# Kernel optimization log

Measured on AMD Instinct MI355X. Metric: run time of the kernel, lower is better.

Reference implementation:

```python
import math
import jax, jax.numpy as jnp
import numpy as np

EMBED_DIM = 1024
NUM_HEADS = 16
HEAD_DIM = EMBED_DIM // NUM_HEADS
B, S = 4, 2048


def setup_inputs() -> dict:
    key = jax.random.key(0)
    ks = jax.random.split(key, 12)
    sc = 1.0 / math.sqrt(EMBED_DIM)
    inp = {
        "query": jax.random.normal(ks[0], (B, S, EMBED_DIM), jnp.float32),
        "key": jax.random.normal(ks[1], (B, S, EMBED_DIM), jnp.float32),
        "value": jax.random.normal(ks[2], (B, S, EMBED_DIM), jnp.float32),
        # causal mask: True = masked (upper triangle above diagonal)
        "attn_mask": jnp.triu(jnp.ones((S, S), jnp.bool_), k=1),
        "q_w": jax.random.normal(ks[3], (EMBED_DIM, EMBED_DIM), jnp.float32) * sc,
        "q_b": jax.random.normal(ks[4], (EMBED_DIM,), jnp.float32) * sc,
        "k_w": jax.random.normal(ks[5], (EMBED_DIM, EMBED_DIM), jnp.float32) * sc,
        "k_b": jax.random.normal(ks[6], (EMBED_DIM,), jnp.float32) * sc,
        "v_w": jax.random.normal(ks[7], (EMBED_DIM, EMBED_DIM), jnp.float32) * sc,
        "v_b": jax.random.normal(ks[8], (EMBED_DIM,), jnp.float32) * sc,
        "o_w": jax.random.normal(ks[9], (EMBED_DIM, EMBED_DIM), jnp.float32) * sc,
        "o_b": jax.random.normal(ks[10], (EMBED_DIM,), jnp.float32) * sc,
    }
    return inp


def _split_heads(x):
    # (B, S, E) -> (B, H, S, D)
    b, s, _ = x.shape
    return x.reshape(b, s, NUM_HEADS, HEAD_DIM).transpose(0, 2, 1, 3)


def reference(query, key, value, attn_mask, q_w, q_b, k_w, k_b, v_w, v_b, o_w, o_b):
    # torch Linear: y = x @ W.T + b
    q = _split_heads(query @ q_w.T + q_b)
    k = _split_heads(key @ k_w.T + k_b)
    v = _split_heads(value @ v_w.T + v_b)
    scale = math.sqrt(HEAD_DIM)
    scores = jnp.einsum("bhqd,bhkd->bhqk", q, k) / scale
    scores = jnp.where(attn_mask[None, None, :, :], -jnp.inf, scores)
    attn = jax.nn.softmax(scores, axis=-1)
    ctx = jnp.einsum("bhqk,bhkd->bhqd", attn, v)  # (B,H,S,D)
    ctx = ctx.transpose(0, 2, 1, 3).reshape(query.shape[0], query.shape[1], EMBED_DIM)
    return ctx @ o_w.T + o_b
```

## Files before the change

kernel.cpp:

```cpp
#include <hip/hip_runtime.h>
#include <stdint.h>

#define BB 4
#define SS 2048
#define EE 1024
#define HH 16
#define DD 64
#define MM (BB*SS)

typedef unsigned short u16;
typedef __attribute__((ext_vector_type(8))) short bf16x8;
typedef __attribute__((ext_vector_type(4))) float f32x4;

#define MFMA __builtin_amdgcn_mfma_f32_16x16x32_bf16

#if __has_builtin(__builtin_amdgcn_exp2f)
#define EXP2(x) __builtin_amdgcn_exp2f(x)
#else
#define EXP2(x) exp2f(x)
#endif

__device__ __forceinline__ u16 f2bf(float f) {
  union { float f; uint32_t u; } x; x.f = f;
  uint32_t r = (x.u + 0x7fffu + ((x.u >> 16) & 1u)) >> 16;
  return (u16)r;
}

__device__ __forceinline__ uint32_t cvtpk(float lo, float hi) {
  uint32_t r;
  asm volatile("v_cvt_pk_bf16_f32 %0, %1, %2" : "=v"(r) : "v"(lo), "v"(hi));
  return r;
}

__device__ __forceinline__ void gl_lds16(const void* g, void* l) {
  __builtin_amdgcn_global_load_lds(
      (const __attribute__((address_space(1))) uint32_t*)g,
      (__attribute__((address_space(3))) uint32_t*)l, 16, 0, 0);
}

__global__ __launch_bounds__(256) void cast_w(
    const float* __restrict__ s0, const float* __restrict__ s1,
    const float* __restrict__ s2, const float* __restrict__ s3,
    u16* __restrict__ d0, u16* __restrict__ d1,
    u16* __restrict__ d2, u16* __restrict__ d3) {
  int i = blockIdx.x * 256 + threadIdx.x;
  int sel = i >> 17, off = i & ((1 << 17) - 1);
  const float* s = sel == 0 ? s0 : sel == 1 ? s1 : sel == 2 ? s2 : s3;
  u16* d = sel == 0 ? d0 : sel == 1 ? d1 : sel == 2 ? d2 : d3;
  const float4* sp = (const float4*)s;
  float4 a = sp[off*2], b = sp[off*2+1];
  union { u16 h[8]; uint4 v; } o;
  o.h[0]=f2bf(a.x); o.h[1]=f2bf(a.y); o.h[2]=f2bf(a.z); o.h[3]=f2bf(a.w);
  o.h[4]=f2bf(b.x); o.h[5]=f2bf(b.y); o.h[6]=f2bf(b.z); o.h[7]=f2bf(b.w);
  *(uint4*)(d + (size_t)off*8) = o.v;
}

template<int A_FP32, int OUT_BF16>
__device__ __forceinline__ void gemm_body(
    const void* __restrict__ Ap, const u16* __restrict__ W,
    const float* __restrict__ bias, void* __restrict__ Cout,
    int Ndim, int Kdim, float scale, int m0, int n0,
    char* AsB, char* BsB) {
  const int tid = threadIdx.x;
  const int lane = tid & 63, w = tid >> 6;
  const int wr = w >> 1, wc = w & 1;
  const int l15 = lane & 15, l4 = lane >> 4;

  f32x4 acc[4][4] = {};

  const int br = tid >> 3, bsl = tid & 7;
  const int ar = tid >> 4, asl = tid & 15;

  auto stage = [&](int k0) {
    if (A_FP32) {
      const float* Af = (const float*)Ap;
      #pragma unroll
      for (int i = 0; i < 8; ++i) {
        int row = i*16 + ar;
        int ss = asl ^ (row & 7);
        gl_lds16(Af + (size_t)(m0 + row)*Kdim + k0 + ss*4, AsB + i*4096 + tid*16);
      }
    } else {
      const u16* Ah = (const u16*)Ap;
      #pragma unroll
      for (int i = 0; i < 4; ++i) {
        int row = i*32 + br;
        int ss = bsl ^ (row & 7);
        gl_lds16(Ah + (size_t)(m0 + row)*Kdim + k0 + ss*8, AsB + i*4096 + tid*16);
      }
    }
    #pragma unroll
    for (int i = 0; i < 4; ++i) {
      int row = i*32 + br;
      int ss = bsl ^ (row & 7);
      gl_lds16(W + (size_t)(n0 + row)*Kdim + k0 + ss*8, BsB + i*4096 + tid*16);
    }
  };

  for (int k0 = 0; k0 < Kdim; k0 += 64) {
    stage(k0);
    __syncthreads();

    bf16x8 af[2][4], bfr[2][4];
    #pragma unroll
    for (int m = 0; m < 4; ++m) {
      int r = wr*64 + m*16 + l15;
      if (A_FP32) {
        const char* rb = AsB + r*256;
        #pragma unroll
        for (int kk = 0; kk < 2; ++kk) {
          f32x4 fa = *(const f32x4*)(rb + (kk*8 + ((l4*2    ) ^ (r & 7)))*16);
          f32x4 fb = *(const f32x4*)(rb + (kk*8 + ((l4*2 + 1) ^ (r & 7)))*16);
          union { uint32_t u[4]; bf16x8 v; } cv;
          cv.u[0] = cvtpk(fa[0], fa[1]);
          cv.u[1] = cvtpk(fa[2], fa[3]);
          cv.u[2] = cvtpk(fb[0], fb[1]);
          cv.u[3] = cvtpk(fb[2], fb[3]);
          af[kk][m] = cv.v;
        }
      } else {
        const char* rb = AsB + r*128;
        #pragma unroll
        for (int kk = 0; kk < 2; ++kk)
          af[kk][m] = *(const bf16x8*)(rb + ((kk*4 + l4) ^ (r & 7))*16);
      }
    }
    #pragma unroll
    for (int n = 0; n < 4; ++n) {
      int rr = wc*64 + n*16 + l15;
      const char* rb = BsB + rr*128;
      #pragma unroll
      for (int kk = 0; kk < 2; ++kk)
        bfr[kk][n] = *(const bf16x8*)(rb + ((kk*4 + l4) ^ (rr & 7))*16);
    }
    #pragma unroll
    for (int kk = 0; kk < 2; ++kk)
      #pragma unroll
      for (int m = 0; m < 4; ++m)
        #pragma unroll
        for (int n = 0; n < 4; ++n)
          acc[m][n] = MFMA(af[kk][m], bfr[kk][n], acc[m][n], 0, 0, 0);
    __syncthreads();
  }

  const int ccol = wc*64 + l15;
  float bv[4];
  #pragma unroll
  for (int n = 0; n < 4; ++n) bv[n] = bias[n0 + ccol + n*16];
  #pragma unroll
  for (int m = 0; m < 4; ++m) {
    #pragma unroll
    for (int i = 0; i < 4; ++i) {
      size_t row = (size_t)(m0 + wr*64 + m*16 + l4*4 + i);
      #pragma unroll
      for (int n = 0; n < 4; ++n) {
        float v = (acc[m][n][i] + bv[n]) * scale;
        size_t idx = row * Ndim + (n0 + ccol + n*16);
        if (OUT_BF16) ((u16*)Cout)[idx] = f2bf(v);
        else          ((float*)Cout)[idx] = v;
      }
    }
  }
}

__global__ __launch_bounds__(256, 2) void gemm_qkv(
    const float* __restrict__ qx, const float* __restrict__ kx, const float* __restrict__ vx,
    const u16* __restrict__ wqm, const u16* __restrict__ wkm, const u16* __restrict__ wvm,
    const float* __restrict__ qbv, const float* __restrict__ kbv, const float* __restrict__ vbv,
    u16* __restrict__ qo, u16* __restrict__ ko, u16* __restrict__ vo) {
  __shared__ alignas(16) char AsB[32768];
  __shared__ alignas(16) char BsB[16384];
  const int flat = blockIdx.x + blockIdx.y * 8 + blockIdx.z * 512;
  const int j = flat & 7, s = flat >> 3;
  const int c = 6*j + (s >> 5), i = s & 31;
  const int nx = i & 7;
  const int my = ((c & 15) << 2) + (i >> 3);
  const int z = c >> 4;
  const float* A = z == 0 ? qx : z == 1 ? kx : vx;
  const u16* W = z == 0 ? wqm : z == 1 ? wkm : wvm;
  const float* bias = z == 0 ? qbv : z == 1 ? kbv : vbv;
  u16* C = z == 0 ? qo : z == 1 ? ko : vo;
  const float scale = z == 0 ? 0.125f : 1.0f;
  gemm_body<1,1>(A, W, bias, C, EE, EE, scale, my * 128, nx * 128, AsB, BsB);
}

__global__ __launch_bounds__(256, 4) void gemm_out(
    const u16* __restrict__ A, const u16* __restrict__ W,
    const float* __restrict__ bias, float* __restrict__ Cout) {
  __shared__ alignas(16) char AsB[16384];
  __shared__ alignas(16) char BsB[16384];
  const int flat = blockIdx.x + blockIdx.y * 8;
  const int j = flat & 7, s = flat >> 3;
  const int nx = s & 7, yy = (j << 3) + (s >> 3);
  gemm_body<0,0>(A, W, bias, Cout, EE, EE, 1.0f, yy * 128, nx * 128, AsB, BsB);
}

__global__ __launch_bounds__(256, 2) void attn10(
    const u16* __restrict__ Q, const u16* __restrict__ K,
    const u16* __restrict__ V, u16* __restrict__ ctx) {
  __shared__ alignas(16) u16 Ks[2][2][64*64];
  __shared__ alignas(16) u16 VTs[2][2][64*64];
  __shared__ alignas(16) u16 Ps[4][32*64];

  const int tid = threadIdx.x, lane = tid & 63, w = tid >> 6;
  const int l15 = lane & 15, l4 = lane >> 4;

  const int f = blockIdx.x;
  const int j = f & 7, s = f >> 3;
  const int qlo = s & 7;
  const int panel = j * 8 + (s >> 3);
  const int h = panel & 15, b = panel >> 4;
  const size_t base = ((size_t)b * SS) * EE + h * DD;

  const int kr  = tid >> 3;
  const int ksl = tid & 7;
  const int rv  = tid >> 2;
  const int vc  = tid & 3;

  u16* KsE  = (u16*)Ks;
  u16* VTsE = (u16*)VTs;
  u16* PsE  = (u16*)Ps + w * 2048;

  auto stageK = [&](int t, int pb, int sub) {
    #pragma unroll
    for (int i = 0; i < 2; ++i) {
      int row = i*32 + kr;
      gl_lds16(K + base + (size_t)(t*64 + row)*EE + (ksl ^ (row & 7))*8,
               KsE + pb*8192 + sub*4096 + i*2048 + tid*8);
    }
  };
  auto vtWrite = [&](int pb, int sub, bf16x8 v0, bf16x8 v1) {
    #pragma unroll
    for (int jj = 0; jj < 16; ++jj) {
      u16 val = jj < 8 ? (u16)v0[jj] : (u16)v1[jj - 8];
      int d = vc*16 + jj;
      int sl = (rv >> 3) ^ (jj & 7) ^ (vc << 1);
      VTsE[pb*8192 + sub*4096 + d*64 + sl*8 + (rv & 7)] = val;
    }
  };

  #pragma unroll 1
  for (int pass = 0; pass < 2; ++pass) {
    const int qblk = pass == 0 ? (15 - qlo) : qlo;
    const int q0 = qblk * 128, wq = q0 + w * 32;
    const int npairs = qblk + 1;

    bf16x8 qf[2][2];
    #pragma unroll
    for (int G = 0; G < 2; ++G)
      #pragma unroll
      for (int kc = 0; kc < 2; ++kc)
        qf[G][kc] = *(const bf16x8*)(Q + base + (size_t)(wq + G*16 + l15)*EE + kc*32 + l4*8);

    f32x4 o[2][4] = {};
    float lsum[2] = {0.f, 0.f};

    auto computeTile = [&](int t, int pb, int sub) {
      if (wq + 31 < t*64) return;
      const bool g0act = (wq + 15 >= t*64);
      const u16* tileK = KsE + pb*8192 + sub*4096;
      const u16* tileV = VTsE + pb*8192 + sub*4096;

      f32x4 sc[2][4] = {};
      __builtin_amdgcn_s_setprio(1);
      #pragma unroll
      for (int nt = 0; nt < 4; ++nt) {
        int row = nt*16 + l15;
        int sw = row & 7;
        const u16* kb = tileK + row*64;
        bf16x8 kf0 = *(const bf16x8*)(kb + ((l4    ) ^ sw)*8);
        bf16x8 kf1 = *(const bf16x8*)(kb + ((4 + l4) ^ sw)*8);
        sc[1][nt] = MFMA(kf0, qf[1][0], sc[1][nt], 0, 0, 0);
        sc[1][nt] = MFMA(kf1, qf[1][1], sc[1][nt], 0, 0, 0);
        if (g0act) {
          sc[0][nt] = MFMA(kf0, qf[0][0], sc[0][nt], 0, 0, 0);
          sc[0][nt] = MFMA(kf1, qf[0][1], sc[0][nt], 0, 0, 0);
        }
      }
      __builtin_amdgcn_s_setprio(0);

      #pragma unroll
      for (int G = 0; G < 2; ++G) {
        if (G == 0 && !g0act) continue;
        const bool nomask = (t*64 + 63 <= wq + G*16);
        const int qg = wq + G*16 + l15;
        #pragma unroll
        for (int nt = 0; nt < 4; ++nt) {
          float p0 = EXP2(__builtin_fmaf(sc[G][nt][0], 1.44269504f, -17.3123405f));
          float p1 = EXP2(__builtin_fmaf(sc[G][nt][1], 1.44269504f, -17.3123405f));
          float p2 = EXP2(__builtin_fmaf(sc[G][nt][2], 1.44269504f, -17.3123405f));
          float p3 = EXP2(__builtin_fmaf(sc[G][nt][3], 1.44269504f, -17.3123405f));
          if (!nomask) {
            int kvs = t*64 + nt*16 + l4*4;
            if (kvs + 0 > qg) p0 = 0.f;
            if (kvs + 1 > qg) p1 = 0.f;
            if (kvs + 2 > qg) p2 = 0.f;
            if (kvs + 3 > qg) p3 = 0.f;
          }
          lsum[G] += (p0 + p1) + (p2 + p3);
          uint2 pk;
          pk.x = cvtpk(p0, p1);
          pk.y = cvtpk(p2, p3);
          *(uint2*)((char*)PsE + (G*16 + l15)*128
                        + (((nt*2 + (l4 >> 1)) ^ (l15 & 7)) * 16)
                        + (l4 & 1) * 8) = pk;
        }
      }

      __builtin_amdgcn_s_setprio(1);
      #pragma unroll
      for (int cc = 0; cc < 2; ++cc) {
        bf16x8 pf1 = *(const bf16x8*)((char*)PsE + (16 + l15)*128
                                     + (((cc*4 + l4) ^ (l15 & 7)) * 16));
        bf16x8 pf0;
        if (g0act)
          pf0 = *(const bf16x8*)((char*)PsE + l15*128
                                     + (((cc*4 + l4) ^ (l15 & 7)) * 16));
        #pragma unroll
        for (int dm = 0; dm < 4; ++dm) {
          int sl = (cc*4 + l4) ^ (l15 & 7) ^ (dm << 1);
          bf16x8 vfv = *(const bf16x8*)(tileV + (dm*16 + l15)*64 + sl*8);
          o[1][dm] = MFMA(pf1, vfv, o[1][dm], 0, 0, 0);
          if (g0act) o[0][dm] = MFMA(pf0, vfv, o[0][dm], 0, 0, 0);
        }
      }
      __builtin_amdgcn_s_setprio(0);
    };

    {
      const u16* va = V + base + (size_t)rv*EE + vc*16;
      const u16* vb = V + base + (size_t)(64 + rv)*EE + vc*16;
      bf16x8 a0 = *(const bf16x8*)va, a1 = *(const bf16x8*)(va + 8);
      bf16x8 b0 = *(const bf16x8*)vb, b1 = *(const bf16x8*)(vb + 8);
      stageK(0, 0, 0);
      stageK(1, 0, 1);
      vtWrite(0, 0, a0, a1);
      vtWrite(0, 1, b0, b1);
    }
    __syncthreads();

    for (int u = 0; u < npairs; ++u) {
      const int cur = u & 1;
      const bool havenext = (u + 1 < npairs);
      bf16x8 na0, na1, nb0, nb1;
      if (havenext) {
        const u16* va = V + base + (size_t)((2*u+2)*64 + rv)*EE + vc*16;
        const u16* vb = V + base + (size_t)((2*u+3)*64 + rv)*EE + vc*16;
        na0 = *(const bf16x8*)va; na1 = *(const bf16x8*)(va + 8);
        nb0 = *(const bf16x8*)vb; nb1 = *(const bf16x8*)(vb + 8);
        stageK(2*u+2, cur ^ 1, 0);
        stageK(2*u+3, cur ^ 1, 1);
      }

      computeTile(2*u, cur, 0);
      if (havenext) vtWrite(cur ^ 1, 0, na0, na1);
      computeTile(2*u + 1, cur, 1);
      if (havenext) vtWrite(cur ^ 1, 1, nb0, nb1);
      __syncthreads();
    }

    #pragma unroll
    for (int G = 0; G < 2; ++G) {
      float r = lsum[G];
      r += __shfl_xor(r, 16);
      r += __shfl_xor(r, 32);
      lsum[G] = 1.0f / r;
    }

    #pragma unroll
    for (int G = 0; G < 2; ++G)
      #pragma unroll
      for (int i = 0; i < 4; ++i) {
        float invv = __shfl(lsum[G], l4*4 + i);
        size_t roff = base + (size_t)(wq + G*16 + l4*4 + i) * EE;
        #pragma unroll
        for (int dm = 0; dm < 4; ++dm)
          ctx[roff + dm*16 + l15] = f2bf(o[G][dm][i] * invv);
      }
  }
}

extern "C" void kernel_launch(void* const* d_in, const int* in_sizes, int n_in,
                              void* d_out, int out_size, void* d_ws, size_t ws_size,
                              hipStream_t stream) {
  const float* query = (const float*)d_in[0];
  const float* key   = (const float*)d_in[1];
  const float* value = (const float*)d_in[2];
  const float* q_w = (const float*)d_in[4];
  const float* q_b = (const float*)d_in[5];
  const float* k_w = (const float*)d_in[6];
  const float* k_b = (const float*)d_in[7];
  const float* v_w = (const float*)d_in[8];
  const float* v_b = (const float*)d_in[9];
  const float* o_w = (const float*)d_in[10];
  const float* o_b = (const float*)d_in[11];

  char* ws = (char*)d_ws;
  const size_t XB = (size_t)MM * EE * 2;
  const size_t WB = (size_t)EE * EE * 2;
  u16* wq = (u16*)(ws);
  u16* wk = (u16*)(ws + WB);
  u16* wv = (u16*)(ws + 2*WB);
  u16* wo = (u16*)(ws + 3*WB);
  u16* qp = (u16*)(ws + 4*WB);
  u16* kp = (u16*)(ws + 4*WB + XB);
  u16* vp = (u16*)(ws + 4*WB + 2*XB);
  u16* ctxb = (u16*)(ws + 4*WB + 3*XB);

  const int nw8 = EE * EE / 8;
  cast_w<<<4*nw8/256, 256, 0, stream>>>(q_w, k_w, v_w, o_w, wq, wk, wv, wo);

  gemm_qkv<<<dim3(8, 64, 3), 256, 0, stream>>>(
      query, key, value, wq, wk, wv, q_b, k_b, v_b, qp, kp, vp);

  attn10<<<512, 256, 0, stream>>>(qp, kp, vp, ctxb);

  gemm_out<<<dim3(EE/128, MM/128), 256, 0, stream>>>(ctxb, wo, o_b, (float*)d_out);
}
```

Before: 164.2 us.

## Load GEMM A operand directly from global into registers, bypassing LDS

The GEMM body no longer stages the A tile through shared memory. Each wave reads its A rows straight from global memory into registers, converting to bf16 where needed, and only the weight tile still goes through LDS. Launch bounds are adjusted for the smaller LDS footprint. The aim is to cut LDS usage and traffic and to raise occupancy, at the cost of duplicated and less-coalesced global reads of A across waves and no async prefetch.

```diff
diff --git a/kernel.cpp b/kernel.cpp
--- a/kernel.cpp
+++ b/kernel.cpp
@@ -60,7 +60,7 @@
     const void* __restrict__ Ap, const u16* __restrict__ W,
     const float* __restrict__ bias, void* __restrict__ Cout,
     int Ndim, int Kdim, float scale, int m0, int n0,
-    char* AsB, char* BsB) {
+    char* BsB) {
   const int tid = threadIdx.x;
   const int lane = tid & 63, w = tid >> 6;
   const int wr = w >> 1, wc = w & 1;
@@ -69,26 +69,17 @@
   f32x4 acc[4][4] = {};
 
   const int br = tid >> 3, bsl = tid & 7;
-  const int ar = tid >> 4, asl = tid & 15;
-
-  auto stage = [&](int k0) {
-    if (A_FP32) {
-      const float* Af = (const float*)Ap;
-      #pragma unroll
-      for (int i = 0; i < 8; ++i) {
-        int row = i*16 + ar;
-        int ss = asl ^ (row & 7);
-        gl_lds16(Af + (size_t)(m0 + row)*Kdim + k0 + ss*4, AsB + i*4096 + tid*16);
-      }
-    } else {
-      const u16* Ah = (const u16*)Ap;
-      #pragma unroll
-      for (int i = 0; i < 4; ++i) {
-        int row = i*32 + br;
-        int ss = bsl ^ (row & 7);
-        gl_lds16(Ah + (size_t)(m0 + row)*Kdim + k0 + ss*8, AsB + i*4096 + tid*16);
-      }
-    }
+
+  const float* arf[4];
+  const u16*   arh[4];
+  #pragma unroll
+  for (int m = 0; m < 4; ++m) {
+    size_t r = (size_t)(m0 + wr*64 + m*16 + l15) * Kdim;
+    if (A_FP32) arf[m] = (const float*)Ap + r;
+    else        arh[m] = (const u16*)Ap + r;
+  }
+
+  auto stageB = [&](int k0) {
     #pragma unroll
     for (int i = 0; i < 4; ++i) {
       int row = i*32 + br;
@@ -98,19 +89,16 @@
   };
 
   for (int k0 = 0; k0 < Kdim; k0 += 64) {
-    stage(k0);
-    __syncthreads();
-
-    bf16x8 af[2][4], bfr[2][4];
+    stageB(k0);
+
+    bf16x8 af[2][4];
     #pragma unroll
     for (int m = 0; m < 4; ++m) {
-      int r = wr*64 + m*16 + l15;
       if (A_FP32) {
-        const char* rb = AsB + r*256;
         #pragma unroll
         for (int kk = 0; kk < 2; ++kk) {
-          f32x4 fa = *(const f32x4*)(rb + (kk*8 + ((l4*2    ) ^ (r & 7)))*16);
-          f32x4 fb = *(const f32x4*)(rb + (kk*8 + ((l4*2 + 1) ^ (r & 7)))*16);
+          f32x4 fa = *(const f32x4*)(arf[m] + k0 + kk*32 + l4*8);
+          f32x4 fb = *(const f32x4*)(arf[m] + k0 + kk*32 + l4*8 + 4);
           union { uint32_t u[4]; bf16x8 v; } cv;
           cv.u[0] = cvtpk(fa[0], fa[1]);
           cv.u[1] = cvtpk(fa[2], fa[3]);
@@ -119,12 +107,15 @@
           af[kk][m] = cv.v;
         }
       } else {
-        const char* rb = AsB + r*128;
         #pragma unroll
         for (int kk = 0; kk < 2; ++kk)
-          af[kk][m] = *(const bf16x8*)(rb + ((kk*4 + l4) ^ (r & 7))*16);
-      }
-    }
+          af[kk][m] = *(const bf16x8*)(arh[m] + k0 + kk*32 + l4*8);
+      }
+    }
+
+    __syncthreads();
+
+    bf16x8 bfr[2][4];
     #pragma unroll
     for (int n = 0; n < 4; ++n) {
       int rr = wc*64 + n*16 + l15;
@@ -163,12 +154,11 @@
   }
 }
 
-__global__ __launch_bounds__(256, 2) void gemm_qkv(
+__global__ __launch_bounds__(256, 3) void gemm_qkv(
     const float* __restrict__ qx, const float* __restrict__ kx, const float* __restrict__ vx,
     const u16* __restrict__ wqm, const u16* __restrict__ wkm, const u16* __restrict__ wvm,
     const float* __restrict__ qbv, const float* __restrict__ kbv, const float* __restrict__ vbv,
     u16* __restrict__ qo, u16* __restrict__ ko, u16* __restrict__ vo) {
-  __shared__ alignas(16) char AsB[32768];
   __shared__ alignas(16) char BsB[16384];
   const int flat = blockIdx.x + blockIdx.y * 8 + blockIdx.z * 512;
   const int j = flat & 7, s = flat >> 3;
@@ -181,18 +171,17 @@
   const float* bias = z == 0 ? qbv : z == 1 ? kbv : vbv;
   u16* C = z == 0 ? qo : z == 1 ? ko : vo;
   const float scale = z == 0 ? 0.125f : 1.0f;
-  gemm_body<1,1>(A, W, bias, C, EE, EE, scale, my * 128, nx * 128, AsB, BsB);
-}
-
-__global__ __launch_bounds__(256, 4) void gemm_out(
+  gemm_body<1,1>(A, W, bias, C, EE, EE, scale, my * 128, nx * 128, BsB);
+}
+
+__global__ __launch_bounds__(256, 2) void gemm_out(
     const u16* __restrict__ A, const u16* __restrict__ W,
     const float* __restrict__ bias, float* __restrict__ Cout) {
-  __shared__ alignas(16) char AsB[16384];
   __shared__ alignas(16) char BsB[16384];
   const int flat = blockIdx.x + blockIdx.y * 8;
   const int j = flat & 7, s = flat >> 3;
   const int nx = s & 7, yy = (j << 3) + (s >> 3);
-  gemm_body<0,0>(A, W, bias, Cout, EE, EE, 1.0f, yy * 128, nx * 128, AsB, BsB);
+  gemm_body<0,0>(A, W, bias, Cout, EE, EE, 1.0f, yy * 128, nx * 128, BsB);
 }
 
 __global__ __launch_bounds__(256, 2) void attn10(
```

Result: slower. 329.1 us (+100.3%).
